# Kernel tuning notes

Measured on AMD Instinct MI355X. Metric: run time of the kernel, lower is better.

## Reference

```python
import jax, jax.numpy as jnp
import numpy as np

EPS = 1e-12  # F.normalize default eps


def _l2_normalize(x, axis):
    n = jnp.sqrt(jnp.sum(x * x, axis=axis, keepdims=True))
    return x / jnp.maximum(n, EPS)


def setup_inputs() -> dict:
    key = jax.random.key(0)
    k1, k2 = jax.random.split(key)
    code = jax.random.normal(k1, (8, 768, 32, 32), dtype=jnp.float32)
    clusters = jax.random.normal(k2, (64, 768), dtype=jnp.float32)
    return {"code": code, "clusters": clusters, "image_hw": 512}


def reference(code, clusters, image_hw):
    # L2-normalize cluster centroids over channel dim and features over C
    normed_clusters = _l2_normalize(clusters, axis=1)            # [N, C]
    normed_features = _l2_normalize(code, axis=1)                # [B, C, H, W]
    # cosine similarity to every cluster
    inner_products = jnp.einsum('bchw,nc->bnhw', normed_features, normed_clusters)  # [B,N,H,W]
    # hard nearest-cluster assignment -> one-hot over N (channel axis 1)
    assign = jnp.argmax(inner_products, axis=1)                  # [B, H, W] int
    n_classes = clusters.shape[0]
    cluster_probs = jnp.moveaxis(
        jax.nn.one_hot(assign, n_classes, dtype=jnp.float32), -1, 1)  # [B,N,H,W]
    # training loss: negative mean of selected (max) similarity
    cluster_loss = -jnp.mean(jnp.sum(cluster_probs * inner_products, axis=1))
    # resize_to(cluster_probs, image): bilinear upsample to image resolution
    B, N = cluster_probs.shape[0], cluster_probs.shape[1]
    resized = jax.image.resize(cluster_probs, (B, N, image_hw, image_hw), method='bilinear')
    return (cluster_loss, resized, code)
```

## Files before the change

kernel.cpp:

```cpp
#include <hip/hip_runtime.h>

#define CCH 768
#define NCL 64
#define HWIN 1024
#define RES_ELEMS 134217728LL
#define CODE_ELEMS 6291456LL
#define CQUADS 1572863LL
#define COPY_BLOCKS 1536
#define DENSE_BLOCKS 4096

typedef float vfloat4 __attribute__((ext_vector_type(4)));

__global__ __launch_bounds__(256) void k_norm(const float* __restrict__ clusters,
                                              const float* __restrict__ code,
                                              float* __restrict__ nc_t,
                                              float* __restrict__ out)
{
    int tid = threadIdx.x;
    int n = blockIdx.x;
    __shared__ float red[256];
    float v0 = clusters[n * CCH + tid];
    float v1 = clusters[n * CCH + tid + 256];
    float v2 = clusters[n * CCH + tid + 512];
    red[tid] = v0 * v0 + v1 * v1 + v2 * v2;
    __syncthreads();
    for (int off = 128; off > 0; off >>= 1) {
        if (tid < off) red[tid] += red[tid + off];
        __syncthreads();
    }
    float scale = 1.0f / fmaxf(sqrtf(red[0]), 1e-12f);
    nc_t[(tid      ) * NCL + n] = v0 * scale;
    nc_t[(tid + 256) * NCL + n] = v1 * scale;
    nc_t[(tid + 512) * NCL + n] = v2 * scale;
    if (n == 0 && tid == 0) {
        out[0] = 0.0f;
        out[RES_ELEMS + 1] = code[0];
        out[RES_ELEMS + 2] = code[1];
        out[RES_ELEMS + 3] = code[2];
        out[RES_ELEMS + CODE_ELEMS] = code[CODE_ELEMS - 1];
    }
}

__global__ __launch_bounds__(256) void k_assign(const float* __restrict__ code,
                                                const float* __restrict__ nc_t,
                                                int* __restrict__ assign,
                                                float* __restrict__ out)
{
    __shared__ float lds_nc[64 * 64];
    __shared__ float lds_red[8 * 2048];
    __shared__ float lds_sq[8 * 32];

    int tid = threadIdx.x;
    int blk = blockIdx.x;
    int cg = tid >> 5;
    int ng = (tid >> 3) & 3;
    int pg = tid & 7;
    int b = blk >> 5;
    int pixb = (blk & 31) << 5;
    const float* codeB = code + (size_t)b * CCH * HWIN + pixb + (pg << 2);

    float acc[4][16];
    #pragma unroll
    for (int p = 0; p < 4; ++p)
        #pragma unroll
        for (int q = 0; q < 16; ++q) acc[p][q] = 0.f;
    float sq0 = 0.f, sq1 = 0.f, sq2 = 0.f, sq3 = 0.f;

    for (int k = 0; k < 12; ++k) {
        __syncthreads();
        const float4* src = (const float4*)(nc_t + k * 4096);
        float4* dst = (float4*)lds_nc;
        #pragma unroll
        for (int i = 0; i < 4; ++i) dst[tid + 256 * i] = src[tid + 256 * i];
        __syncthreads();
        #pragma unroll
        for (int m = 0; m < 8; ++m) {
            int ch = k * 64 + cg * 8 + m;
            float4 f = *(const float4*)(codeB + ch * HWIN);
            sq0 += f.x * f.x; sq1 += f.y * f.y; sq2 += f.z * f.z; sq3 += f.w * f.w;
            const float* ncrow = lds_nc + ((cg * 8 + m) << 6) + (ng << 4);
            #pragma unroll
            for (int q = 0; q < 16; ++q) {
                float w = ncrow[q];
                acc[0][q] += f.x * w;
                acc[1][q] += f.y * w;
                acc[2][q] += f.z * w;
                acc[3][q] += f.w * w;
            }
        }
    }

    #pragma unroll
    for (int p = 0; p < 4; ++p) {
        float4* dstp = (float4*)&lds_red[cg * 2048 + (pg * 4 + p) * 64 + ng * 16];
        dstp[0] = make_float4(acc[p][0],  acc[p][1],  acc[p][2],  acc[p][3]);
        dstp[1] = make_float4(acc[p][4],  acc[p][5],  acc[p][6],  acc[p][7]);
        dstp[2] = make_float4(acc[p][8],  acc[p][9],  acc[p][10], acc[p][11]);
        dstp[3] = make_float4(acc[p][12], acc[p][13], acc[p][14], acc[p][15]);
    }
    if (ng == 0) {
        lds_sq[cg * 32 + pg * 4 + 0] = sq0;
        lds_sq[cg * 32 + pg * 4 + 1] = sq1;
        lds_sq[cg * 32 + pg * 4 + 2] = sq2;
        lds_sq[cg * 32 + pg * 4 + 3] = sq3;
    }
    __syncthreads();

    for (int idx = tid; idx < 2048; idx += 256) {
        float s = 0.f;
        #pragma unroll
        for (int c2 = 0; c2 < 8; ++c2) s += lds_red[c2 * 2048 + idx];
        lds_nc[idx] = s;
    }
    __syncthreads();

    if (tid < 32) {
        float ss = 0.f;
        #pragma unroll
        for (int c2 = 0; c2 < 8; ++c2) ss += lds_sq[c2 * 32 + tid];
        float inv = 1.0f / fmaxf(sqrtf(ss), 1e-12f);
        float best = -1e30f; int bi = 0;
        for (int n = 0; n < 64; ++n) {
            float v = lds_nc[tid * 64 + n];
            if (v > best) { best = v; bi = n; }
        }
        assign[blk * 32 + tid] = bi;
        float l = best * inv;
        l += __shfl_down(l, 16);
        l += __shfl_down(l, 8);
        l += __shfl_down(l, 4);
        l += __shfl_down(l, 2);
        l += __shfl_down(l, 1);
        if (tid == 0) atomicAdd(out, -l * (1.0f / 8192.0f));
    }
}

__global__ __launch_bounds__(256) void k_dense(const int* __restrict__ assign,
                                               const float* __restrict__ code,
                                               float* __restrict__ out)
{
    int tid = threadIdx.x;
    int blk = blockIdx.x;

    if (blk >= DENSE_BLOCKS) {
        long long u = (long long)(blk - DENSE_BLOCKS) * 256 + tid;
        #pragma unroll
        for (int k = 0; k < 4; ++k) {
            long long q = u + (long long)k * (COPY_BLOCKS * 256);
            if (q < CQUADS) {
                const float* src = code + 3 + 4 * q;
                vfloat4 v;
                v.x = __builtin_nontemporal_load(src + 0);
                v.y = __builtin_nontemporal_load(src + 1);
                v.z = __builtin_nontemporal_load(src + 2);
                v.w = __builtin_nontemporal_load(src + 3);
                __builtin_nontemporal_store(v, (vfloat4*)(out + RES_ELEMS + 4 + 4 * q));
            }
        }
        return;
    }

    int b = blk >> 9;
    int i = blk & 511;
    __shared__ int   s_r0[32], s_r1[32];
    __shared__ int4  s_ids[128];
    __shared__ float4 s_fj[128];

    float xi = (i + 0.5f) * 0.0625f - 0.5f;
    float fif = floorf(xi);
    int ii = (int)fif;
    float fi = xi - fif;
    int i0 = ii < 0 ? 0 : ii;
    int i1 = (ii + 1) > 31 ? 31 : (ii + 1);

    if (tid < 32) {
        s_r0[tid] = assign[(b << 10) + (i0 << 5) + tid];
        s_r1[tid] = assign[(b << 10) + (i1 << 5) + tid];
    }
    __syncthreads();

    if (tid < 128) {
        int s = tid;
        int4 ids; float4 fj4;
        int jl[4];
        if (s == 0) { jl[0] = 0; jl[1] = 1; jl[2] = 2; jl[3] = 511; }
        else { jl[0] = 4 * s - 1; jl[1] = 4 * s; jl[2] = 4 * s + 1; jl[3] = 4 * s + 2; }
        int pk[4]; float fjv[4];
        #pragma unroll
        for (int k = 0; k < 4; ++k) {
            int j = jl[k];
            float xj = (j + 0.5f) * 0.0625f - 0.5f;
            float fjf = floorf(xj);
            int jj = (int)fjf;
            fjv[k] = xj - fjf;
            int j0 = jj < 0 ? 0 : jj;
            int j1 = (jj + 1) > 31 ? 31 : (jj + 1);
            pk[k] = s_r0[j0] | (s_r0[j1] << 8) | (s_r1[j0] << 16) | (s_r1[j1] << 24);
        }
        ids.x = pk[0]; ids.y = pk[1]; ids.z = pk[2]; ids.w = pk[3];
        fj4.x = fjv[0]; fj4.y = fjv[1]; fj4.z = fjv[2]; fj4.w = fjv[3];
        s_ids[s] = ids;
        s_fj[s] = fj4;
    }
    __syncthreads();

    float fi1 = 1.0f - fi;
    long long rowoff = 1LL + ((long long)b << 24) + ((long long)i << 9);

    #pragma unroll 4
    for (int it = 0; it < 32; ++it) {
        int task = it * 256 + tid;
        int n = task >> 7;
        int s = task & 127;
        int4 p4 = s_ids[s];
        float4 f4 = s_fj[s];
        float v[4];
        int pks[4] = { p4.x, p4.y, p4.z, p4.w };
        float fjs[4] = { f4.x, f4.y, f4.z, f4.w };
        #pragma unroll
        for (int k = 0; k < 4; ++k) {
            int p = pks[k];
            float P = (((p      ) & 255) == n ? fi1 : 0.f)
                    + (((p >> 16) & 255) == n ? fi  : 0.f);
            float Q = (((p >>  8) & 255) == n ? fi1 : 0.f)
                    + (((p >> 24) & 255) == n ? fi  : 0.f);
            v[k] = P + fjs[k] * (Q - P);
        }
        float* rowbase = out + rowoff + ((long long)n << 18);
        if (s == 0) {
            __builtin_nontemporal_store(v[0], rowbase + 0);
            __builtin_nontemporal_store(v[1], rowbase + 1);
            __builtin_nontemporal_store(v[2], rowbase + 2);
            __builtin_nontemporal_store(v[3], rowbase + 511);
        } else {
            vfloat4 vv; vv.x = v[0]; vv.y = v[1]; vv.z = v[2]; vv.w = v[3];
            __builtin_nontemporal_store(vv, (vfloat4*)(rowbase + 4 * s - 1));
        }
    }
}

extern "C" void kernel_launch(void* const* d_in, const int* in_sizes, int n_in,
                              void* d_out, int out_size, void* d_ws, size_t ws_size,
                              hipStream_t stream)
{
    const float* code     = (const float*)d_in[0];
    const float* clusters = (const float*)d_in[1];
    float* out = (float*)d_out;
    float* nc_t = (float*)d_ws;
    int* assign = (int*)((char*)d_ws + 196608);

    k_norm  <<<NCL,                       256, 0, stream>>>(clusters, code, nc_t, out);
    k_assign<<<256,                       256, 0, stream>>>(code, nc_t, assign, out);
    k_dense <<<DENSE_BLOCKS + COPY_BLOCKS, 256, 0, stream>>>(assign, code, out);
}
```

Baseline: 651.1 us.

## Remap dense upsample blocks to per-plane row chunks using ballot bitmasks

The dense resize kernel now assigns each block one (batch, cluster, 128-row chunk) instead of one output row across all 64 clusters. Per-cluster membership of the needed source rows is turned into bitmasks with wave ballots, and each thread writes rows within a single contiguous output plane. The aim is more sequential write streams and cheaper per-element bit tests than byte-packed comparisons. Nontemporal loads and stores are also swapped for plain ones, which can change cache behaviour on the large write-only output.

```diff
diff --git a/kernel.cpp b/kernel.cpp
--- a/kernel.cpp
+++ b/kernel.cpp
@@ -7,9 +7,7 @@
 #define CODE_ELEMS 6291456LL
 #define CQUADS 1572863LL
 #define COPY_BLOCKS 1536
-#define DENSE_BLOCKS 4096
-
-typedef float vfloat4 __attribute__((ext_vector_type(4)));
+#define DENSE_BLOCKS 2048
 
 __global__ __launch_bounds__(256) void k_norm(const float* __restrict__ clusters,
                                               const float* __restrict__ code,
@@ -149,43 +147,47 @@
             long long q = u + (long long)k * (COPY_BLOCKS * 256);
             if (q < CQUADS) {
                 const float* src = code + 3 + 4 * q;
-                vfloat4 v;
-                v.x = __builtin_nontemporal_load(src + 0);
-                v.y = __builtin_nontemporal_load(src + 1);
-                v.z = __builtin_nontemporal_load(src + 2);
-                v.w = __builtin_nontemporal_load(src + 3);
-                __builtin_nontemporal_store(v, (vfloat4*)(out + RES_ELEMS + 4 + 4 * q));
+                float4 v = make_float4(src[0], src[1], src[2], src[3]);
+                *(float4*)(out + RES_ELEMS + 4 + 4 * q) = v;
             }
         }
         return;
     }
 
-    int b = blk >> 9;
-    int i = blk & 511;
-    __shared__ int   s_r0[32], s_r1[32];
-    __shared__ int4  s_ids[128];
+    int b =  blk >> 8;
+    int n = (blk >> 2) & 63;
+    int c =  blk & 3;
+    int I0 = c << 7;
+    int rbase = (I0 >> 4) - 1;
+
+    __shared__ unsigned s_mask[10];
+    __shared__ int4   s_jj[128];
     __shared__ float4 s_fj[128];
 
-    float xi = (i + 0.5f) * 0.0625f - 0.5f;
-    float fif = floorf(xi);
-    int ii = (int)fif;
-    float fi = xi - fif;
-    int i0 = ii < 0 ? 0 : ii;
-    int i1 = (ii + 1) > 31 ? 31 : (ii + 1);
-
-    if (tid < 32) {
-        s_r0[tid] = assign[(b << 10) + (i0 << 5) + tid];
-        s_r1[tid] = assign[(b << 10) + (i1 << 5) + tid];
-    }
-    __syncthreads();
+    int lane = tid & 63;
+    int w = tid >> 6;
+
+    {
+        int r = (w << 1) + (lane >> 5);
+        int ir = rbase + r; ir = ir < 0 ? 0 : (ir > 31 ? 31 : ir);
+        bool pred = assign[(b << 10) + (ir << 5) + (lane & 31)] == n;
+        unsigned long long m = __ballot(pred);
+        if (lane == 0) { s_mask[(w << 1)] = (unsigned)m; s_mask[(w << 1) + 1] = (unsigned)(m >> 32); }
+    }
+    if (w == 0) {
+        int r = 8 + (lane >> 5);
+        int ir = rbase + r; ir = ir < 0 ? 0 : (ir > 31 ? 31 : ir);
+        bool pred = assign[(b << 10) + (ir << 5) + (lane & 31)] == n;
+        unsigned long long m = __ballot(pred);
+        if (lane == 0) { s_mask[8] = (unsigned)m; s_mask[9] = (unsigned)(m >> 32); }
+    }
 
     if (tid < 128) {
         int s = tid;
-        int4 ids; float4 fj4;
         int jl[4];
         if (s == 0) { jl[0] = 0; jl[1] = 1; jl[2] = 2; jl[3] = 511; }
         else { jl[0] = 4 * s - 1; jl[1] = 4 * s; jl[2] = 4 * s + 1; jl[3] = 4 * s + 2; }
-        int pk[4]; float fjv[4];
+        int pj[4]; float fjv[4];
         #pragma unroll
         for (int k = 0; k < 4; ++k) {
             int j = jl[k];
@@ -195,46 +197,48 @@
             fjv[k] = xj - fjf;
             int j0 = jj < 0 ? 0 : jj;
             int j1 = (jj + 1) > 31 ? 31 : (jj + 1);
-            pk[k] = s_r0[j0] | (s_r0[j1] << 8) | (s_r1[j0] << 16) | (s_r1[j1] << 24);
-        }
-        ids.x = pk[0]; ids.y = pk[1]; ids.z = pk[2]; ids.w = pk[3];
-        fj4.x = fjv[0]; fj4.y = fjv[1]; fj4.z = fjv[2]; fj4.w = fjv[3];
-        s_ids[s] = ids;
-        s_fj[s] = fj4;
-    }
-    __syncthreads();
-
-    float fi1 = 1.0f - fi;
-    long long rowoff = 1LL + ((long long)b << 24) + ((long long)i << 9);
-
-    #pragma unroll 4
-    for (int it = 0; it < 32; ++it) {
-        int task = it * 256 + tid;
-        int n = task >> 7;
-        int s = task & 127;
-        int4 p4 = s_ids[s];
-        float4 f4 = s_fj[s];
+            pj[k] = j0 | (j1 << 8);
+        }
+        s_jj[s] = make_int4(pj[0], pj[1], pj[2], pj[3]);
+        s_fj[s] = make_float4(fjv[0], fjv[1], fjv[2], fjv[3]);
+    }
+    __syncthreads();
+
+    int rr = tid >> 7;
+    int s  = tid & 127;
+    int4   pj4 = s_jj[s];
+    float4 fj4 = s_fj[s];
+    int   j0a[4] = { pj4.x & 255, pj4.y & 255, pj4.z & 255, pj4.w & 255 };
+    int   j1a[4] = { pj4.x >> 8,  pj4.y >> 8,  pj4.z >> 8,  pj4.w >> 8 };
+    float fja[4] = { fj4.x, fj4.y, fj4.z, fj4.w };
+
+    long long planebase = 1LL + ((long long)b << 24) + ((long long)n << 18);
+
+    for (int r2 = 0; r2 < 64; ++r2) {
+        int i = I0 + (r2 << 1) + rr;
+        float xi = (i + 0.5f) * 0.0625f - 0.5f;
+        float fif = floorf(xi);
+        int ii = (int)fif;
+        float fi = xi - fif;
+        float fi1 = 1.0f - fi;
+        unsigned m0 = s_mask[ii - rbase];
+        unsigned m1 = s_mask[ii - rbase + 1];
         float v[4];
-        int pks[4] = { p4.x, p4.y, p4.z, p4.w };
-        float fjs[4] = { f4.x, f4.y, f4.z, f4.w };
         #pragma unroll
         for (int k = 0; k < 4; ++k) {
-            int p = pks[k];
-            float P = (((p      ) & 255) == n ? fi1 : 0.f)
-                    + (((p >> 16) & 255) == n ? fi  : 0.f);
-            float Q = (((p >>  8) & 255) == n ? fi1 : 0.f)
-                    + (((p >> 24) & 255) == n ? fi  : 0.f);
-            v[k] = P + fjs[k] * (Q - P);
-        }
-        float* rowbase = out + rowoff + ((long long)n << 18);
+            float b00 = (float)((m0 >> j0a[k]) & 1u);
+            float b01 = (float)((m0 >> j1a[k]) & 1u);
+            float b10 = (float)((m1 >> j0a[k]) & 1u);
+            float b11 = (float)((m1 >> j1a[k]) & 1u);
+            float P = fi1 * b00 + fi * b10;
+            float Q = fi1 * b01 + fi * b11;
+            v[k] = P + fja[k] * (Q - P);
+        }
+        float* rowbase = out + planebase + ((long long)i << 9);
         if (s == 0) {
-            __builtin_nontemporal_store(v[0], rowbase + 0);
-            __builtin_nontemporal_store(v[1], rowbase + 1);
-            __builtin_nontemporal_store(v[2], rowbase + 2);
-            __builtin_nontemporal_store(v[3], rowbase + 511);
+            rowbase[0] = v[0]; rowbase[1] = v[1]; rowbase[2] = v[2]; rowbase[511] = v[3];
         } else {
-            vfloat4 vv; vv.x = v[0]; vv.y = v[1]; vv.z = v[2]; vv.w = v[3];
-            __builtin_nontemporal_store(vv, (vfloat4*)(rowbase + 4 * s - 1));
+            *(float4*)(rowbase + 4 * s - 1) = make_float4(v[0], v[1], v[2], v[3]);
         }
     }
 }
@@ -249,7 +253,7 @@
     float* nc_t = (float*)d_ws;
     int* assign = (int*)((char*)d_ws + 196608);
 
-    k_norm  <<<NCL,                       256, 0, stream>>>(clusters, code, nc_t, out);
-    k_assign<<<256,                       256, 0, stream>>>(code, nc_t, assign, out);
+    k_norm  <<<NCL,                        256, 0, stream>>>(clusters, code, nc_t, out);
+    k_assign<<<256,                        256, 0, stream>>>(code, nc_t, assign, out);
     k_dense <<<DENSE_BLOCKS + COPY_BLOCKS, 256, 0, stream>>>(assign, code, out);
 }
```

Result: faster. 618.6 us (-5.0%).
